# Performance work log

Measured on AMD Instinct MI355X. Metric: run time of the kernel, lower is better.

## Reference

```python
import jax, jax.numpy as jnp
import numpy as np
import math

D = 2048
N_HEADS = 16
D_HEAD = D // N_HEADS
B = 2
L = 2048


def _rope_tables(seq_len, d_head, base=10000.0):
    # standard half-rotation RoPE tables, shape [L, d_head]
    inv_freq = 1.0 / (base ** (jnp.arange(0, d_head, 2, dtype=jnp.float32) / d_head))
    ang = jnp.arange(seq_len, dtype=jnp.float32)[:, None] * inv_freq[None, :]  # [L, d_head/2]
    cos = jnp.concatenate([jnp.cos(ang), jnp.cos(ang)], axis=-1)  # [L, d_head]
    sin = jnp.concatenate([jnp.sin(ang), jnp.sin(ang)], axis=-1)
    return cos, sin


def _apply_rope(x, cos, sin):
    # x: [B, H, L, d_head]; rotate_half convention
    half = x.shape[-1] // 2
    x_rot = jnp.concatenate([-x[..., half:], x[..., :half]], axis=-1)
    return x * cos[None, None, :, :] + x_rot * sin[None, None, :, :]


def setup_inputs() -> dict:
    key = jax.random.key(0)
    k1, k2, k3 = jax.random.split(key, 3)
    x = jax.random.normal(k1, (B, L, D), dtype=jnp.float32)
    w_qkv = jax.random.normal(k2, (D, 3 * D), dtype=jnp.float32) * (1.0 / math.sqrt(D))
    w_out = jax.random.normal(k3, (D, D), dtype=jnp.float32) * (1.0 / math.sqrt(D))
    s_qk = jnp.asarray(math.sqrt(D_HEAD), dtype=jnp.float32)  # init sqrt(d_head)
    return {"x": x, "w_qkv": w_qkv, "w_out": w_out, "s_qk": s_qk}


def reference(x, w_qkv, w_out, s_qk):
    Bs, Ls, Ds = x.shape
    qkv = jnp.einsum("bld,de->ble", x, w_qkv).reshape(Bs, Ls, 3, N_HEADS, D_HEAD)
    q, k, v = qkv[:, :, 0], qkv[:, :, 1], qkv[:, :, 2]
    # -> [B, H, L, d_head]
    q = jnp.transpose(q, (0, 2, 1, 3))
    k = jnp.transpose(k, (0, 2, 1, 3))
    v = jnp.transpose(v, (0, 2, 1, 3))
    cos, sin = _rope_tables(Ls, D_HEAD)
    q = _apply_rope(q, cos, sin)
    k = _apply_rope(k, cos, sin)
    # L2-normalize per head (torch F.normalize eps=1e-12)
    q = q / jnp.maximum(jnp.linalg.norm(q, axis=-1, keepdims=True), 1e-12)
    k = k / jnp.maximum(jnp.linalg.norm(k, axis=-1, keepdims=True), 1e-12)
    # softmax((q*s_qk) @ k^T) with causal mask, scale=1.0
    scores = jnp.einsum("bhqd,bhkd->bhqk", q * s_qk, k)
    causal = jnp.tril(jnp.ones((Ls, Ls), dtype=bool))
    scores = jnp.where(causal[None, None, :, :], scores, -jnp.inf)
    attn = jax.nn.softmax(scores, axis=-1)
    out = jnp.einsum("bhqk,bhkd->bhqd", attn, v)
    out = jnp.transpose(out, (0, 2, 1, 3)).reshape(Bs, Ls, Ds)
    return jnp.einsum("bld,de->ble", out, w_out)
```

## Files before the change

kernel.cpp:

```cpp
#include <hip/hip_runtime.h>
#include <math.h>


#define D 2048
#define NH 16
#define DH 128
#define BB 2
#define LL 2048
#define BHD (BB*NH)
#define MROWS (BB*LL)
#define KDIM D

typedef __attribute__((ext_vector_type(8))) short short8;
typedef __attribute__((ext_vector_type(4))) float floatx4;

__device__ __forceinline__ unsigned short f2bf(float f) {
    unsigned u = __float_as_uint(f);
    unsigned r = u + 0x7FFFu + ((u >> 16) & 1u);
    return (unsigned short)(r >> 16);
}
__device__ __forceinline__ float bf2f(unsigned short u) {
    return __uint_as_float(((unsigned)u) << 16);
}

__device__ __forceinline__ void async16(const void* g, void* lds) {
    __builtin_amdgcn_global_load_lds(
        (const __attribute__((address_space(1))) unsigned int*)g,
        (__attribute__((address_space(3))) unsigned int*)lds, 16, 0, 0);
}

template<int CTRL>
__device__ __forceinline__ float dpp_movf(float x) {
    return __int_as_float(__builtin_amdgcn_update_dpp(
        0, __float_as_int(x), CTRL, 0xF, 0xF, true));
}
__device__ __forceinline__ float row_max16(float x) {
    x = fmaxf(x, dpp_movf<0xB1>(x));
    x = fmaxf(x, dpp_movf<0x4E>(x));
    x = fmaxf(x, dpp_movf<0x124>(x));
    x = fmaxf(x, dpp_movf<0x128>(x));
    return x;
}
__device__ __forceinline__ float row_sum16(float x) {
    x += dpp_movf<0xB1>(x);
    x += dpp_movf<0x4E>(x);
    x += dpp_movf<0x124>(x);
    x += dpp_movf<0x128>(x);
    return x;
}

__global__ __launch_bounds__(256)
void cast_bf16_r14(const float* __restrict__ in,
                   unsigned short* __restrict__ out, int n4)
{
    int i = blockIdx.x * 256 + threadIdx.x;
    if (i < n4) {
        float4 v = ((const float4*)in)[i];
        ushort4 o;
        o.x = f2bf(v.x); o.y = f2bf(v.y); o.z = f2bf(v.z); o.w = f2bf(v.w);
        ((ushort4*)out)[i] = o;
    }
}

__global__ __launch_bounds__(256)
void transpose_cast_r14(const float* __restrict__ W,
                        unsigned short* __restrict__ Wt, int K, int N)
{
    __shared__ float tile[32][33];
    const int tx = threadIdx.x & 31, ty = threadIdx.x >> 5;
    const int n0 = blockIdx.x * 32, k0 = blockIdx.y * 32;
#pragma unroll
    for (int r = 0; r < 4; r++)
        tile[ty + 8 * r][tx] = W[(size_t)(k0 + ty + 8 * r) * N + n0 + tx];
    __syncthreads();
#pragma unroll
    for (int r = 0; r < 4; r++)
        Wt[(size_t)(n0 + ty + 8 * r) * K + k0 + tx] = f2bf(tile[tx][ty + 8 * r]);
}

__global__ __launch_bounds__(256)
void transpose_v_r14(const unsigned short* __restrict__ Vb,
                     unsigned short* __restrict__ VtG)
{
    __shared__ unsigned short tile[32][34];
    const int tx = threadIdx.x & 31, ty = threadIdx.x >> 5;
    const int l0 = blockIdx.x * 32, d0 = blockIdx.y * 32;
    const int bh = blockIdx.z;
    const unsigned short* src = Vb + (size_t)bh * LL * DH;
    unsigned short* dst = VtG + (size_t)bh * DH * LL;
#pragma unroll
    for (int r = 0; r < 4; r++)
        tile[ty + 8 * r][tx] = src[(size_t)(l0 + ty + 8 * r) * DH + d0 + tx];
    __syncthreads();
#pragma unroll
    for (int r = 0; r < 4; r++)
        dst[(size_t)(d0 + ty + 8 * r) * LL + l0 + tx] = tile[tx][ty + 8 * r];
}

template<int N, int MODE>
__global__ __launch_bounds__(256)
void gemm_mfma_r14(const unsigned short* __restrict__ A,
                   const unsigned short* __restrict__ Bt,
                   float* __restrict__ C, unsigned short* __restrict__ Qo,
                   unsigned short* __restrict__ Ko, unsigned short* __restrict__ Vo)
{
    __shared__ unsigned short As[128 * 32];
    __shared__ unsigned short Bs[128 * 32];
    const int t = threadIdx.x;
    const int w = t >> 6, lane = t & 63;
    const int lrow = lane & 15, quad = lane >> 4;
    const int m0 = blockIdx.y * 128, n0 = blockIdx.x * 128;
    const int wm = (w >> 1) * 64, wn = (w & 1) * 64;

    floatx4 acc[4][4];
#pragma unroll
    for (int i = 0; i < 4; i++)
#pragma unroll
        for (int j = 0; j < 4; j++) acc[i][j] = (floatx4){0.f, 0.f, 0.f, 0.f};

    const int srow = 32 * w + (lane >> 2);
    const int sseg = (lane & 3) * 8;

    for (int k0 = 0; k0 < KDIM; k0 += 32) {
        __syncthreads();
        async16(&A [(size_t)(m0 + srow)      * KDIM + k0 + sseg], &As[(32 * w)      * 32]);
        async16(&A [(size_t)(m0 + srow + 16) * KDIM + k0 + sseg], &As[(32 * w + 16) * 32]);
        async16(&Bt[(size_t)(n0 + srow)      * KDIM + k0 + sseg], &Bs[(32 * w)      * 32]);
        async16(&Bt[(size_t)(n0 + srow + 16) * KDIM + k0 + sseg], &Bs[(32 * w + 16) * 32]);
        __syncthreads();

        short8 a[4], b[4];
#pragma unroll
        for (int i = 0; i < 4; i++)
            a[i] = *(const short8*)&As[(wm + i * 16 + lrow) * 32 + quad * 8];
#pragma unroll
        for (int j = 0; j < 4; j++)
            b[j] = *(const short8*)&Bs[(wn + j * 16 + lrow) * 32 + quad * 8];
#pragma unroll
        for (int i = 0; i < 4; i++)
#pragma unroll
            for (int j = 0; j < 4; j++)
                acc[i][j] = __builtin_amdgcn_mfma_f32_16x16x32_bf16(a[i], b[j], acc[i][j], 0, 0, 0);
    }

    if (MODE == 0) {
#pragma unroll
        for (int i = 0; i < 4; i++)
#pragma unroll
            for (int j = 0; j < 4; j++) {
                int col = n0 + wn + j * 16 + lrow;
#pragma unroll
                for (int r = 0; r < 4; r++) {
                    int m = m0 + wm + i * 16 + quad * 4 + r;
                    C[(size_t)m * N + col] = acc[i][j][r];
                }
            }
    } else {
        const int s = n0 >> 11;
        const int h = (n0 & 2047) >> 7;
        unsigned short* dst = (s == 0) ? Qo : (s == 1) ? Ko : Vo;
#pragma unroll
        for (int i = 0; i < 4; i++)
#pragma unroll
            for (int j = 0; j < 4; j++) {
                int dh = wn + j * 16 + lrow;
#pragma unroll
                for (int r = 0; r < 4; r++) {
                    int m = m0 + wm + i * 16 + quad * 4 + r;
                    int b = m >> 11, l = m & 2047;
                    dst[(((size_t)b * NH + h) * LL + l) * DH + dh] = f2bf(acc[i][j][r]);
                }
            }
    }
}

__global__ __launch_bounds__(256)
void rope_norm_r14(unsigned short* __restrict__ Q,
                   unsigned short* __restrict__ K,
                   const float* __restrict__ s_qk_ptr)
{
    const int wid  = threadIdx.x >> 6;
    const int lane = threadIdx.x & 63;
    const int row  = blockIdx.x * 4 + wid;
    const int l    = row & (LL - 1);
    const size_t base = (size_t)row * DH;

    float ang = (float)l * expf(-0.14391157f * (float)lane);
    float c = cosf(ang), s = sinf(ang);

    float qlo = bf2f(Q[base + lane]), qhi = bf2f(Q[base + lane + 64]);
    float klo = bf2f(K[base + lane]), khi = bf2f(K[base + lane + 64]);

    float qr_lo = fmaf(qlo, c, (-qhi) * s);
    float qr_hi = fmaf(qhi, c,   qlo  * s);
    float kr_lo = fmaf(klo, c, (-khi) * s);
    float kr_hi = fmaf(khi, c,   klo  * s);

    float qs = qr_lo * qr_lo + qr_hi * qr_hi;
    float ks = kr_lo * kr_lo + kr_hi * kr_hi;
    qs = row_sum16(qs);  ks = row_sum16(ks);
    qs += __shfl_xor(qs, 16);  ks += __shfl_xor(ks, 16);
    qs += __shfl_xor(qs, 32);  ks += __shfl_xor(ks, 32);
    float qn = fmaxf(sqrtf(qs), 1e-12f);
    float kn = fmaxf(sqrtf(ks), 1e-12f);

    float sqk = s_qk_ptr[0];
    Q[base + lane]      = f2bf(qr_lo / qn * sqk);
    Q[base + lane + 64] = f2bf(qr_hi / qn * sqk);
    K[base + lane]      = f2bf(kr_lo / kn);
    K[base + lane + 64] = f2bf(kr_hi / kn);
}

#define ABQ 128
#define ABK 64
__global__ __launch_bounds__(256, 2)
void attn_mfma_r14(const unsigned short* __restrict__ Q,
                   const unsigned short* __restrict__ K,
                   const unsigned short* __restrict__ Vt,
                   unsigned short* __restrict__ AOb)
{
    __shared__ __align__(16) unsigned short Ks[2][ABK * DH];
    __shared__ __align__(16) unsigned short Vs[2][DH * ABK];
    __shared__ __align__(16) unsigned short Ps[4][32][64];

    const int t = threadIdx.x;
    const int w = t >> 6, lane = t & 63;
    const int lrow = lane & 15, quad = lane >> 4;
    const int bh = blockIdx.x;
    const int y  = blockIdx.y;
    const int qt = (y < 8) ? (15 - y) : (y - 8);
    const int q0 = qt * ABQ;
    const int qw = q0 + w * 32;

    const unsigned short* Qb = Q  + (size_t)bh * LL * DH;
    const unsigned short* Kb = K  + (size_t)bh * LL * DH;
    const unsigned short* Vg = Vt + (size_t)bh * DH * LL;

    short8 aq[2][4];
#pragma unroll
    for (int h = 0; h < 2; h++)
#pragma unroll
        for (int kk = 0; kk < 4; kk++)
            aq[h][kk] = *(const short8*)&Qb[(size_t)(qw + 16 * h + lrow) * DH
                                            + kk * 32 + quad * 8];

    floatx4 oacc[2][8];
#pragma unroll
    for (int h = 0; h < 2; h++)
#pragma unroll
        for (int dt = 0; dt < 8; dt++) oacc[h][dt] = (floatx4){0.f, 0.f, 0.f, 0.f};
    float mrow[2][4], lsum[2][4];
#pragma unroll
    for (int h = 0; h < 2; h++)
#pragma unroll
        for (int r = 0; r < 4; r++) { mrow[h][r] = -1e30f; lsum[h][r] = 0.f; }

    auto STAGE = [&](int tile, int buf) {
        const int k0s = tile * ABK;
#pragma unroll
        for (int c = 0; c < 4; c++) {
            int row = 16 * w + 4 * c;
            int r   = row + (lane >> 4);
            int col = (lane & 15) ^ (r & 7);
            async16(&Kb[(size_t)(k0s + r) * DH + col * 8], &Ks[buf][row * DH]);
        }
#pragma unroll
        for (int c = 0; c < 4; c++) {
            int row = 32 * w + 8 * c;
            int r   = row + (lane >> 3);
            int col = (lane & 7) ^ (r & 7);
            async16(&Vg[(size_t)r * LL + k0s + col * 8], &Vs[buf][row * ABK]);
        }
    };

    const int ntiles = 2 * qt + 2;
    STAGE(0, 0);
    __syncthreads();

    int cur = 0;
    for (int tile = 0; tile < ntiles; tile++) {
        const int k0 = tile * ABK;
        if (tile + 1 < ntiles) STAGE(tile + 1, cur ^ 1);

        floatx4 sacc[2][4];
#pragma unroll
        for (int h = 0; h < 2; h++)
#pragma unroll
            for (int j = 0; j < 4; j++) sacc[h][j] = (floatx4){0.f, 0.f, 0.f, 0.f};
        __builtin_amdgcn_s_setprio(1);
#pragma unroll
        for (int kk = 0; kk < 4; kk++) {
#pragma unroll
            for (int j = 0; j < 4; j++) {
                int slot = (kk * 4 + quad) ^ (lrow & 7);
                short8 bk = *(const short8*)&Ks[cur][(j * 16 + lrow) * DH + slot * 8];
                sacc[0][j] = __builtin_amdgcn_mfma_f32_16x16x32_bf16(aq[0][kk], bk, sacc[0][j], 0, 0, 0);
                sacc[1][j] = __builtin_amdgcn_mfma_f32_16x16x32_bf16(aq[1][kk], bk, sacc[1][j], 0, 0, 0);
            }
        }
        __builtin_amdgcn_s_setprio(0);

#pragma unroll
        for (int h = 0; h < 2; h++) {
            if (k0 + ABK - 1 > qw + 16 * h) {
#pragma unroll
                for (int j = 0; j < 4; j++) {
                    int key = k0 + j * 16 + lrow;
#pragma unroll
                    for (int r = 0; r < 4; r++) {
                        int q = qw + 16 * h + quad * 4 + r;
                        if (key > q) sacc[h][j][r] = -1e30f;
                    }
                }
            }
        }

#pragma unroll
        for (int h = 0; h < 2; h++) {
            float alpha[4];
#pragma unroll
            for (int r = 0; r < 4; r++) {
                float mt = fmaxf(fmaxf(sacc[h][0][r], sacc[h][1][r]),
                                 fmaxf(sacc[h][2][r], sacc[h][3][r]));
                mt = row_max16(mt);
                float mn = fmaxf(mrow[h][r], mt);
                alpha[r] = __expf(mrow[h][r] - mn);
                mrow[h][r] = mn;
            }
#pragma unroll
            for (int r = 0; r < 4; r++) {
                int rowp = 16 * h + quad * 4 + r;
                float rs = 0.f;
#pragma unroll
                for (int j = 0; j < 4; j++) {
                    float p = __expf(sacc[h][j][r] - mrow[h][r]);
                    rs += p;
                    int slot = (2 * j + (lrow >> 3)) ^ (rowp & 7);
                    Ps[w][rowp][slot * 8 + (lrow & 7)] = f2bf(p);
                }
                rs = row_sum16(rs);
                lsum[h][r] = lsum[h][r] * alpha[r] + rs;
            }
#pragma unroll
            for (int dt = 0; dt < 8; dt++)
#pragma unroll
                for (int r = 0; r < 4; r++) oacc[h][dt][r] *= alpha[r];
        }

        __builtin_amdgcn_s_setprio(1);
#pragma unroll
        for (int kk2 = 0; kk2 < 2; kk2++) {
            int pslot = (kk2 * 4 + quad) ^ (lrow & 7);
            short8 pa0 = *(const short8*)&Ps[w][lrow][pslot * 8];
            short8 pa1 = *(const short8*)&Ps[w][16 + lrow][pslot * 8];
#pragma unroll
            for (int dt = 0; dt < 8; dt++) {
                int slot = (kk2 * 4 + quad) ^ (lrow & 7);
                short8 bv = *(const short8*)&Vs[cur][(dt * 16 + lrow) * ABK + slot * 8];
                oacc[0][dt] = __builtin_amdgcn_mfma_f32_16x16x32_bf16(pa0, bv, oacc[0][dt], 0, 0, 0);
                oacc[1][dt] = __builtin_amdgcn_mfma_f32_16x16x32_bf16(pa1, bv, oacc[1][dt], 0, 0, 0);
            }
        }
        __builtin_amdgcn_s_setprio(0);

        __syncthreads();
        cur ^= 1;
    }

    const int b = bh >> 4, hd = bh & 15;
#pragma unroll
    for (int h = 0; h < 2; h++)
#pragma unroll
        for (int r = 0; r < 4; r++) {
            float inv = 1.f / lsum[h][r];
            int q = qw + 16 * h + quad * 4 + r;
            size_t base = ((size_t)b * LL + q) * D + hd * DH;
#pragma unroll
            for (int dt = 0; dt < 8; dt++)
                AOb[base + dt * 16 + lrow] = f2bf(oacc[h][dt][r] * inv);
        }
}

extern "C" void kernel_launch(void* const* d_in, const int* in_sizes, int n_in,
                              void* d_out, int out_size, void* d_ws, size_t ws_size,
                              hipStream_t stream)
{
    const float* x     = (const float*)d_in[0];
    const float* w_qkv = (const float*)d_in[1];
    const float* w_out = (const float*)d_in[2];
    const float* s_qk  = (const float*)d_in[3];
    float* out = (float*)d_out;

    const size_t SZ = (size_t)BB * NH * LL * DH;
    unsigned short* u = (unsigned short*)d_ws;
    unsigned short* xb    = u;
    unsigned short* wqkvT = xb    + (size_t)MROWS * KDIM;
    unsigned short* woutT = wqkvT + (size_t)(3 * D) * KDIM;
    unsigned short* Qb    = woutT + (size_t)D * KDIM;
    unsigned short* Kb    = Qb + SZ;
    unsigned short* Vb    = Kb + SZ;
    unsigned short* VtG   = Vb + SZ;

    cast_bf16_r14<<<(MROWS * KDIM / 4 + 255) / 256, 256, 0, stream>>>(
        x, xb, MROWS * KDIM / 4);
    transpose_cast_r14<<<dim3(3 * D / 32, KDIM / 32), 256, 0, stream>>>(
        w_qkv, wqkvT, KDIM, 3 * D);
    gemm_mfma_r14<3 * D, 1><<<dim3(3 * D / 128, MROWS / 128), 256, 0, stream>>>(
        xb, wqkvT, nullptr, Qb, Kb, Vb);
    rope_norm_r14<<<dim3(BHD * LL / 4), 256, 0, stream>>>(Qb, Kb, s_qk);
    transpose_v_r14<<<dim3(LL / 32, DH / 32, BHD), 256, 0, stream>>>(Vb, VtG);
    attn_mfma_r14<<<dim3(BHD, LL / ABQ), 256, 0, stream>>>(Qb, Kb, VtG, xb);
    transpose_cast_r14<<<dim3(D / 32, D / 32), 256, 0, stream>>>(
        w_out, woutT, D, D);
    gemm_mfma_r14<D, 0><<<dim3(D / 128, MROWS / 128), 256, 0, stream>>>(
        xb, woutT, out, nullptr, nullptr, nullptr);
}
```

Measured before the change: 419.6 us.

## Fuse V transpose into QKV GEMM, remap blocks per XCD, defer softmax rescale

The QKV GEMM epilogue now writes V directly in transposed [d_head, L] layout with packed 4-element stores, which removes the separate V transpose kernel and its extra buffer pass. GEMM blocks are remapped so consecutive M tiles land on the same XCD, aiming at better L2 reuse of the weight tiles. In attention, the online softmax skips the max update and the output rescale whenever the whole wave's new row max rises by no more than 8 over the running max. P is also written to LDS as packed 32-bit pairs using DPP exchanges. Deferring the rescale relies on bounded scores and is exact, but adds branching and wave votes.

After: 454.0 us. +8.2%, slower.

```diff
diff --git a/kernel.cpp b/kernel.cpp
--- a/kernel.cpp
+++ b/kernel.cpp
@@ -50,7 +50,7 @@
 }
 
 __global__ __launch_bounds__(256)
-void cast_bf16_r14(const float* __restrict__ in,
+void cast_bf16_r15(const float* __restrict__ in,
                    unsigned short* __restrict__ out, int n4)
 {
     int i = blockIdx.x * 256 + threadIdx.x;
@@ -63,7 +63,7 @@
 }
 
 __global__ __launch_bounds__(256)
-void transpose_cast_r14(const float* __restrict__ W,
+void transpose_cast_r15(const float* __restrict__ W,
                         unsigned short* __restrict__ Wt, int K, int N)
 {
     __shared__ float tile[32][33];
@@ -78,28 +78,9 @@
         Wt[(size_t)(n0 + ty + 8 * r) * K + k0 + tx] = f2bf(tile[tx][ty + 8 * r]);
 }
 
-__global__ __launch_bounds__(256)
-void transpose_v_r14(const unsigned short* __restrict__ Vb,
-                     unsigned short* __restrict__ VtG)
-{
-    __shared__ unsigned short tile[32][34];
-    const int tx = threadIdx.x & 31, ty = threadIdx.x >> 5;
-    const int l0 = blockIdx.x * 32, d0 = blockIdx.y * 32;
-    const int bh = blockIdx.z;
-    const unsigned short* src = Vb + (size_t)bh * LL * DH;
-    unsigned short* dst = VtG + (size_t)bh * DH * LL;
-#pragma unroll
-    for (int r = 0; r < 4; r++)
-        tile[ty + 8 * r][tx] = src[(size_t)(l0 + ty + 8 * r) * DH + d0 + tx];
-    __syncthreads();
-#pragma unroll
-    for (int r = 0; r < 4; r++)
-        dst[(size_t)(d0 + ty + 8 * r) * LL + l0 + tx] = tile[tx][ty + 8 * r];
-}
-
 template<int N, int MODE>
 __global__ __launch_bounds__(256)
-void gemm_mfma_r14(const unsigned short* __restrict__ A,
+void gemm_mfma_r15(const unsigned short* __restrict__ A,
                    const unsigned short* __restrict__ Bt,
                    float* __restrict__ C, unsigned short* __restrict__ Qo,
                    unsigned short* __restrict__ Ko, unsigned short* __restrict__ Vo)
@@ -109,7 +90,12 @@
     const int t = threadIdx.x;
     const int w = t >> 6, lane = t & 63;
     const int lrow = lane & 15, quad = lane >> 4;
-    const int m0 = blockIdx.y * 128, n0 = blockIdx.x * 128;
+
+    const int lin = blockIdx.y * gridDim.x + blockIdx.x;
+    const int xcd = lin & 7, idx = lin >> 3;
+    const int m0 = (xcd * 4 + (idx & 3)) * 128;
+    const int n0 = (idx >> 2) * 128;
+
     const int wm = (w >> 1) * 64, wn = (w & 1) * 64;
 
     floatx4 acc[4][4];
@@ -158,24 +144,40 @@
     } else {
         const int s = n0 >> 11;
         const int h = (n0 & 2047) >> 7;
-        unsigned short* dst = (s == 0) ? Qo : (s == 1) ? Ko : Vo;
-#pragma unroll
-        for (int i = 0; i < 4; i++)
-#pragma unroll
-            for (int j = 0; j < 4; j++) {
-                int dh = wn + j * 16 + lrow;
-#pragma unroll
-                for (int r = 0; r < 4; r++) {
-                    int m = m0 + wm + i * 16 + quad * 4 + r;
-                    int b = m >> 11, l = m & 2047;
-                    dst[(((size_t)b * NH + h) * LL + l) * DH + dh] = f2bf(acc[i][j][r]);
+        if (s == 2) {
+#pragma unroll
+            for (int i = 0; i < 4; i++) {
+                int m = m0 + wm + i * 16 + quad * 4;
+                int b = m >> 11, l = m & 2047;
+#pragma unroll
+                for (int j = 0; j < 4; j++) {
+                    int dh = wn + j * 16 + lrow;
+                    ushort4 v;
+                    v.x = f2bf(acc[i][j][0]); v.y = f2bf(acc[i][j][1]);
+                    v.z = f2bf(acc[i][j][2]); v.w = f2bf(acc[i][j][3]);
+                    *(ushort4*)&Vo[(((size_t)b * NH + h) * DH + dh) * LL + l] = v;
                 }
             }
+        } else {
+            unsigned short* dst = (s == 0) ? Qo : Ko;
+#pragma unroll
+            for (int i = 0; i < 4; i++)
+#pragma unroll
+                for (int j = 0; j < 4; j++) {
+                    int dh = wn + j * 16 + lrow;
+#pragma unroll
+                    for (int r = 0; r < 4; r++) {
+                        int m = m0 + wm + i * 16 + quad * 4 + r;
+                        int b = m >> 11, l = m & 2047;
+                        dst[(((size_t)b * NH + h) * LL + l) * DH + dh] = f2bf(acc[i][j][r]);
+                    }
+                }
+        }
     }
 }
 
 __global__ __launch_bounds__(256)
-void rope_norm_r14(unsigned short* __restrict__ Q,
+void rope_norm_r15(unsigned short* __restrict__ Q,
                    unsigned short* __restrict__ K,
                    const float* __restrict__ s_qk_ptr)
 {
@@ -214,7 +216,7 @@
 #define ABQ 128
 #define ABK 64
 __global__ __launch_bounds__(256, 2)
-void attn_mfma_r14(const unsigned short* __restrict__ Q,
+void attn_mfma_r15(const unsigned short* __restrict__ Q,
                    const unsigned short* __restrict__ K,
                    const unsigned short* __restrict__ Vt,
                    unsigned short* __restrict__ AOb)
@@ -315,36 +317,69 @@
             }
         }
 
-#pragma unroll
-        for (int h = 0; h < 2; h++) {
-            float alpha[4];
+        float mt_[2][4];
+#pragma unroll
+        for (int h = 0; h < 2; h++)
 #pragma unroll
             for (int r = 0; r < 4; r++) {
                 float mt = fmaxf(fmaxf(sacc[h][0][r], sacc[h][1][r]),
                                  fmaxf(sacc[h][2][r], sacc[h][3][r]));
-                mt = row_max16(mt);
-                float mn = fmaxf(mrow[h][r], mt);
-                alpha[r] = __expf(mrow[h][r] - mn);
-                mrow[h][r] = mn;
-            }
-#pragma unroll
-            for (int r = 0; r < 4; r++) {
-                int rowp = 16 * h + quad * 4 + r;
-                float rs = 0.f;
-#pragma unroll
-                for (int j = 0; j < 4; j++) {
-                    float p = __expf(sacc[h][j][r] - mrow[h][r]);
-                    rs += p;
-                    int slot = (2 * j + (lrow >> 3)) ^ (rowp & 7);
-                    Ps[w][rowp][slot * 8 + (lrow & 7)] = f2bf(p);
+                mt_[h][r] = row_max16(mt);
+            }
+        bool defer = true;
+#pragma unroll
+        for (int h = 0; h < 2; h++)
+#pragma unroll
+            for (int r = 0; r < 4; r++)
+                defer = defer && (mt_[h][r] - mrow[h][r] <= 8.0f);
+        defer = __all(defer);
+
+        float alpha[2][4];
+        if (!defer) {
+#pragma unroll
+            for (int h = 0; h < 2; h++)
+#pragma unroll
+                for (int r = 0; r < 4; r++) {
+                    float mn = fmaxf(mrow[h][r], mt_[h][r]);
+                    alpha[h][r] = __expf(mrow[h][r] - mn);
+                    mrow[h][r] = mn;
                 }
-                rs = row_sum16(rs);
-                lsum[h][r] = lsum[h][r] * alpha[r] + rs;
-            }
-#pragma unroll
-            for (int dt = 0; dt < 8; dt++)
-#pragma unroll
-                for (int r = 0; r < 4; r++) oacc[h][dt][r] *= alpha[r];
+        }
+
+#pragma unroll
+        for (int r = 0; r < 4; r++) {
+            const int rp0 = quad * 4 + r;
+            const int rowp = (lane & 1) ? (16 + rp0) : rp0;
+            float rs0 = 0.f, rs1 = 0.f;
+#pragma unroll
+            for (int j = 0; j < 4; j++) {
+                float p0 = __expf(sacc[0][j][r] - mrow[0][r]);
+                float p1 = __expf(sacc[1][j][r] - mrow[1][r]);
+                rs0 += p0; rs1 += p1;
+                float n0 = dpp_movf<0xB1>(p0);
+                float n1 = dpp_movf<0xB1>(p1);
+                unsigned pk = (lane & 1)
+                    ? ((unsigned)f2bf(n1) | ((unsigned)f2bf(p1) << 16))
+                    : ((unsigned)f2bf(p0) | ((unsigned)f2bf(n0) << 16));
+                int slot = (2 * j + (lrow >> 3)) ^ (rp0 & 7);
+                *(unsigned*)&Ps[w][rowp][slot * 8 + (lrow & 6)] = pk;
+            }
+            rs0 = row_sum16(rs0); rs1 = row_sum16(rs1);
+            if (defer) {
+                lsum[0][r] += rs0;
+                lsum[1][r] += rs1;
+            } else {
+                lsum[0][r] = lsum[0][r] * alpha[0][r] + rs0;
+                lsum[1][r] = lsum[1][r] * alpha[1][r] + rs1;
+            }
+        }
+        if (!defer) {
+#pragma unroll
+            for (int h = 0; h < 2; h++)
+#pragma unroll
+                for (int dt = 0; dt < 8; dt++)
+#pragma unroll
+                    for (int r = 0; r < 4; r++) oacc[h][dt][r] *= alpha[h][r];
         }
 
         __builtin_amdgcn_s_setprio(1);
@@ -398,20 +433,18 @@
     unsigned short* woutT = wqkvT + (size_t)(3 * D) * KDIM;
     unsigned short* Qb    = woutT + (size_t)D * KDIM;
     unsigned short* Kb    = Qb + SZ;
-    unsigned short* Vb    = Kb + SZ;
-    unsigned short* VtG   = Vb + SZ;
-
-    cast_bf16_r14<<<(MROWS * KDIM / 4 + 255) / 256, 256, 0, stream>>>(
+    unsigned short* VtG   = Kb + SZ;
+
+    cast_bf16_r15<<<(MROWS * KDIM / 4 + 255) / 256, 256, 0, stream>>>(
         x, xb, MROWS * KDIM / 4);
-    transpose_cast_r14<<<dim3(3 * D / 32, KDIM / 32), 256, 0, stream>>>(
+    transpose_cast_r15<<<dim3(3 * D / 32, KDIM / 32), 256, 0, stream>>>(
         w_qkv, wqkvT, KDIM, 3 * D);
-    gemm_mfma_r14<3 * D, 1><<<dim3(3 * D / 128, MROWS / 128), 256, 0, stream>>>(
-        xb, wqkvT, nullptr, Qb, Kb, Vb);
-    rope_norm_r14<<<dim3(BHD * LL / 4), 256, 0, stream>>>(Qb, Kb, s_qk);
-    transpose_v_r14<<<dim3(LL / 32, DH / 32, BHD), 256, 0, stream>>>(Vb, VtG);
-    attn_mfma_r14<<<dim3(BHD, LL / ABQ), 256, 0, stream>>>(Qb, Kb, VtG, xb);
-    transpose_cast_r14<<<dim3(D / 32, D / 32), 256, 0, stream>>>(
+    gemm_mfma_r15<3 * D, 1><<<dim3(3 * D / 128, MROWS / 128), 256, 0, stream>>>(
+        xb, wqkvT, nullptr, Qb, Kb, VtG);
+    rope_norm_r15<<<dim3(BHD * LL / 4), 256, 0, stream>>>(Qb, Kb, s_qk);
+    attn_mfma_r15<<<dim3(BHD, LL / ABQ), 256, 0, stream>>>(Qb, Kb, VtG, xb);
+    transpose_cast_r15<<<dim3(D / 32, D / 32), 256, 0, stream>>>(
         w_out, woutT, D, D);
-    gemm_mfma_r14<D, 0><<<dim3(D / 128, MROWS / 128), 256, 0, stream>>>(
+    gemm_mfma_r15<D, 0><<<dim3(D / 128, MROWS / 128), 256, 0, stream>>>(
         xb, woutT, out, nullptr, nullptr, nullptr);
 }
```
